# Kernel tuning notes

Measured on AMD Instinct MI355X. Metric: run time of the kernel, lower is better.

## Reference

```python
import jax, jax.numpy as jnp
import numpy as np

N = 50000          # num nodes
E = 800000         # num edges (before self loops)
F = 128            # input feature dim
UNITS = 128        # output units
ATT_UNITS = 128    # attention units (Q/K dim)
HEADS = 8


def setup_inputs() -> dict:
    key = jax.random.key(0)
    ks = jax.random.split(key, 6)
    s = 1.0 / np.sqrt(F).astype(np.float32)  # ~glorot scale
    return {
        "x": jax.random.normal(ks[0], (N, F), dtype=jnp.float32),
        "edge_index": jax.random.randint(ks[1], (2, E), 0, N, dtype=jnp.int32),
        "query_kernel": jax.random.normal(ks[2], (F, ATT_UNITS), dtype=jnp.float32) * s,
        "query_bias": jnp.zeros((ATT_UNITS,), jnp.float32),
        "key_kernel": jax.random.normal(ks[3], (F, ATT_UNITS), dtype=jnp.float32) * s,
        "key_bias": jnp.zeros((ATT_UNITS,), jnp.float32),
        "kernel": jax.random.normal(ks[4], (F, UNITS), dtype=jnp.float32) * s,
        "bias": jnp.zeros((UNITS,), jnp.float32),
    }


def segment_softmax(scores, seg, num_segments):
    # scores: [E', H], seg: [E'] -> softmax over edges sharing the same target node, per head
    smax = jax.ops.segment_max(scores, seg, num_segments=num_segments)
    sexp = jnp.exp(scores - smax[seg])
    ssum = jax.ops.segment_sum(sexp, seg, num_segments=num_segments)
    return sexp / ssum[seg]


def reference(x, edge_index, query_kernel, query_bias, key_kernel, key_bias, kernel, bias):
    num_nodes = x.shape[0]
    # add self-loop edges (as in tf_geometric add_self_loop_edge)
    loop = jnp.arange(num_nodes, dtype=edge_index.dtype)
    row = jnp.concatenate([edge_index[0], loop])  # target nodes, [E']
    col = jnp.concatenate([edge_index[1], loop])  # source nodes, [E']

    Q = jax.nn.relu(x @ query_kernel + query_bias)[row]  # [E', A]
    K = jax.nn.relu(x @ key_kernel + key_bias)[col]      # [E', A]
    V = (x @ kernel)[col]                                 # [E', U]

    # split into attention heads: tf.split(..., num_heads, axis=-1)
    Qh = Q.reshape(-1, HEADS, ATT_UNITS // HEADS)
    Kh = K.reshape(-1, HEADS, ATT_UNITS // HEADS)
    att = jnp.sum(Qh * Kh, axis=-1)                       # [E', H]
    alpha = segment_softmax(att, row, num_nodes)          # [E', H]

    # split_value_heads=True: split V into head slices, weight, scatter-add, concat
    Vh = V.reshape(-1, HEADS, UNITS // HEADS)             # [E', H, U/H]
    msg = Vh * alpha[:, :, None]
    out = jax.ops.segment_sum(msg, row, num_segments=num_nodes)  # [N, H, U/H]
    out = out.reshape(num_nodes, UNITS)
    out = out + bias  # use_bias=True, activation=None
    return out
```

## Files before the change

kernel.cpp:

```cpp
#include <hip/hip_runtime.h>
#include <hip/hip_fp16.h>
#include <cstdint>

#define FDIM 128
#define XSTR 136
#define NROWTILE 128
#define WCHUNKS ((FDIM * XSTR * 2) / 1024)
#define XCHUNKS ((NROWTILE * XSTR * 2) / 1024)
#define CSRS 128

typedef __attribute__((ext_vector_type(8))) _Float16 half8;
typedef __attribute__((ext_vector_type(2))) _Float16 h2;
typedef __attribute__((ext_vector_type(16))) float float16;

#if defined(__has_builtin)
#if __has_builtin(__builtin_amdgcn_fdot2)
#define HAVE_FDOT2 1
#endif
#endif

__device__ __forceinline__ void gload_lds16(const void* g, void* s) {
    __builtin_amdgcn_global_load_lds(
        (const __attribute__((address_space(1))) void*)g,
        (__attribute__((address_space(3))) void*)s, 16, 0, 0);
}

__device__ __forceinline__ h2 as_h2(unsigned u) {
    union { unsigned u; h2 h; } c; c.u = u; return c.h;
}
__device__ __forceinline__ float2 h2_to_f2(unsigned u) {
    __half2 h = *(__half2*)&u;
    return __half22float2(h);
}

__global__ __launch_bounds__(256) void edges_k(
    const float* __restrict__ x, __half* __restrict__ XH,
    const int* __restrict__ ei, int E,
    const float* __restrict__ Wq, const float* __restrict__ Wk,
    const float* __restrict__ Wv, __half* __restrict__ WTH,
    int* __restrict__ deg, int* __restrict__ csr, int N, int Npad)
{
    int idx = blockIdx.x * 256 + threadIdx.x;

    if (idx < Npad * 32) {
        int row = idx >> 5;
        int c = (idx & 31) << 2;
        float4 v = make_float4(0.f, 0.f, 0.f, 0.f);
        if (row < N) v = *(const float4*)(x + (size_t)row * FDIM + c);
        __half h[4] = {__float2half_rn(v.x), __float2half_rn(v.y),
                       __float2half_rn(v.z), __float2half_rn(v.w)};
        *(ushort4*)(XH + (size_t)row * XSTR + c) = *(ushort4*)h;
    }

    if (idx < 3 * FDIM * FDIM) {
        int mat = idx >> 14;
        int m = idx & 16383;
        int k = m >> 7;
        int nn = m & 127;
        const float* __restrict__ W = (mat == 0) ? Wq : (mat == 1) ? Wk : Wv;
        WTH[(size_t)mat * FDIM * XSTR + nn * XSTR + k] =
            __float2half_rn(W[k * FDIM + nn]);
    }

    if (idx < E) {
        int row = ei[idx];
        int col = ei[E + idx];
        int slot = atomicAdd(&deg[row], 1);
        if (slot < CSRS) csr[(row << 7) + slot] = col;
    }
}

__global__ __launch_bounds__(256) void gemm_mfma_k(
    const __half* __restrict__ XH, const __half* __restrict__ WTH,
    const float* __restrict__ bq, const float* __restrict__ bk,
    const float* __restrict__ bias,
    __half* __restrict__ Qb, uint2* __restrict__ KV, int N)
{
    __shared__ __half xs[NROWTILE * XSTR];
    __shared__ __half ws[FDIM * XSTR];

    const int tid  = threadIdx.x;
    const int wave = tid >> 6;
    const int lane = tid & 63;
    const int r0   = blockIdx.x * NROWTILE;
    const int mat  = blockIdx.y;

    const char* wbase = (const char*)(WTH + (size_t)mat * FDIM * XSTR);
    for (int c = wave; c < XCHUNKS; c += 4) {
        gload_lds16((const char*)(XH + (size_t)r0 * XSTR) + c * 1024 + lane * 16,
                    (char*)xs + c * 1024);
        gload_lds16(wbase + c * 1024 + lane * 16, (char*)ws + c * 1024);
    }
    __syncthreads();

    const int mrow = lane & 31;
    const int half = lane >> 5;
    const int arow = wave * 32 + mrow;

    float16 acc[4];
    #pragma unroll
    for (int nt = 0; nt < 4; ++nt)
        #pragma unroll
        for (int r = 0; r < 16; ++r) acc[nt][r] = 0.f;

    #pragma unroll
    for (int ks = 0; ks < 8; ++ks) {
        const int ko = ks * 16 + half * 8;
        half8 ah = *(const half8*)(xs + arow * XSTR + ko);
        #pragma unroll
        for (int nt = 0; nt < 4; ++nt) {
            half8 bh = *(const half8*)(ws + (nt * 32 + mrow) * XSTR + ko);
            acc[nt] = __builtin_amdgcn_mfma_f32_32x32x16_f16(ah, bh, acc[nt], 0, 0, 0);
        }
    }

    __syncthreads();

    const float* bvec = (mat == 0) ? bq : (mat == 1) ? bk : bias;
    #pragma unroll
    for (int nt = 0; nt < 4; ++nt) {
        const int col = nt * 32 + mrow;
        const float bb = bvec[col];
        #pragma unroll
        for (int reg = 0; reg < 16; ++reg) {
            int rl = wave * 32 + (reg & 3) + 8 * (reg >> 2) + 4 * half;
            float v = acc[nt][reg] + bb;
            if (mat < 2) v = fmaxf(v, 0.f);
            ws[rl * XSTR + col] = __float2half_rn(v);
        }
    }
    __syncthreads();

    if (mat == 0) {
        #pragma unroll
        for (int it = 0; it < 8; ++it) {
            int idx = it * 256 + tid;
            int row = idx >> 4;
            int c = (idx & 15) * 8;
            uint4 v = *(const uint4*)(ws + row * XSTR + c);
            if (r0 + row < N)
                *(uint4*)(Qb + (size_t)(r0 + row) * FDIM + c) = v;
        }
    } else {
        __half* kvh = (__half*)KV;
        const int sub = (mat == 2) ? 2 : 0;
        #pragma unroll
        for (int it = 0; it < 32; ++it) {
            int idx = it * 256 + tid;
            int row = idx >> 6;
            int p = idx & 63;
            unsigned v = *(const unsigned*)(ws + row * XSTR + 2 * p);
            if (r0 + row < N)
                *(unsigned*)(kvh + (size_t)(r0 + row) * 256 + p * 4 + sub) = v;
        }
    }
}

__global__ __launch_bounds__(256) void aggregate_k(
    const __half* __restrict__ Qb, const uint2* __restrict__ KV,
    const int* __restrict__ deg, const int* __restrict__ csr,
    float* __restrict__ out, int N)
{
    const int lane = threadIdx.x & 63;
    int n = blockIdx.x * 4 + (threadIdx.x >> 6);
    if (n >= N) return;
    n = __builtin_amdgcn_readfirstlane(n);

    int d = __builtin_amdgcn_readfirstlane(deg[n]);
    if (d > CSRS) d = CSRS;
    const int off   = n << 7;
    const int total = d + 1;

    const unsigned qu = *(const unsigned*)(Qb + (size_t)n * FDIM + 2 * lane);
    const h2 q2 = as_h2(qu);
#ifndef HAVE_FDOT2
    const float2 qf = h2_to_f2(qu);
#endif

    float acc0 = 0.f, acc1 = 0.f, lsum = 0.f;

    int idxbuf[8];
    #pragma unroll
    for (int u = 0; u < 8; ++u)
        idxbuf[u] = (u == 0) ? n : ((u < total) ? csr[off + u - 1] : 0);

    for (int t = 0; t < total; t += 8) {
        uint2 kv[8];
        #pragma unroll
        for (int u = 0; u < 8; ++u)
            kv[u] = KV[(((unsigned)idxbuf[u]) << 6) + lane];
        #pragma unroll
        for (int u = 0; u < 8; ++u) {
            int nx = t + 8 + u;
            idxbuf[u] = (nx < total) ? csr[off + nx - 1] : 0;
        }
        #pragma unroll
        for (int u = 0; u < 8; ++u) {
#ifdef HAVE_FDOT2
            float p = __builtin_amdgcn_fdot2(as_h2(kv[u].x), q2, 0.0f, false);
#else
            float2 kf = h2_to_f2(kv[u].x);
            float p = qf.x * kf.x + qf.y * kf.y;
#endif
            p += __shfl_xor(p, 1);
            p += __shfl_xor(p, 2);
            p += __shfl_xor(p, 4);
            float s = (t + u < total) ? __expf(p) : 0.f;
            float2 vf = h2_to_f2(kv[u].y);
            lsum += s;
            acc0 += s * vf.x;
            acc1 += s * vf.y;
        }
    }

    const float inv = 1.0f / lsum;
    float2 o;
    o.x = acc0 * inv;
    o.y = acc1 * inv;
    *(float2*)(out + (size_t)n * FDIM + 2 * lane) = o;
}

extern "C" void kernel_launch(void* const* d_in, const int* in_sizes, int n_in,
                              void* d_out, int out_size, void* d_ws, size_t ws_size,
                              hipStream_t stream)
{
    const float* x    = (const float*)d_in[0];
    const int*   ei   = (const int*)d_in[1];
    const float* Wq   = (const float*)d_in[2];
    const float* bq   = (const float*)d_in[3];
    const float* Wk   = (const float*)d_in[4];
    const float* bk   = (const float*)d_in[5];
    const float* Wv   = (const float*)d_in[6];
    const float* bias = (const float*)d_in[7];
    float* out = (float*)d_out;

    const int N = in_sizes[0] / FDIM;
    const int E = in_sizes[1] / 2;
    const int nblk = (N + NROWTILE - 1) / NROWTILE;
    const int Npad = nblk * NROWTILE;

    __half* WTH = (__half*)d_ws;
    __half* XH  = WTH + (size_t)3 * FDIM * XSTR;
    __half* Qb  = XH + (size_t)Npad * XSTR;
    uint2*  KV  = (uint2*)(Qb + (size_t)N * FDIM);
    int* deg    = (int*)(KV + (size_t)N * 64);
    int* csr    = deg + N;

    (void)hipMemsetAsync(deg, 0, (size_t)N * sizeof(int), stream);

    edges_k<<<(Npad * 32 + 255) / 256, 256, 0, stream>>>(
        x, XH, ei, E, Wq, Wk, Wv, WTH, deg, csr, N, Npad);

    gemm_mfma_k<<<dim3(nblk, 3), 256, 0, stream>>>(
        XH, WTH, bq, bk, bias, Qb, KV, N);

    aggregate_k<<<(N + 3) / 4, 256, 0, stream>>>(Qb, KV, deg, csr, out, N);
}
```

Before: 212.2 us.

## Fuse fp16 conversion of x into GEMM and loop over three weight matrices per block

Removes the separate XH half-precision staging buffer: each GEMM block now loads its fp32 x tile, converts it to fp16 in LDS, and computes Q, K and V in sequence, reloading each weight matrix into shared memory between passes. This reads x once instead of once per projection and drops the global write and readback of XH. In exchange the grid shrinks to a third as many blocks with serialized weight reloads and extra barriers, so there is less parallelism and weight-load latency is not overlapped with compute.

New measurement: 218.5 us. 3.0% more time.

```diff
diff --git a/kernel.cpp b/kernel.cpp
--- a/kernel.cpp
+++ b/kernel.cpp
@@ -6,7 +6,6 @@
 #define XSTR 136
 #define NROWTILE 128
 #define WCHUNKS ((FDIM * XSTR * 2) / 1024)
-#define XCHUNKS ((NROWTILE * XSTR * 2) / 1024)
 #define CSRS 128
 
 typedef __attribute__((ext_vector_type(8))) _Float16 half8;
@@ -34,23 +33,12 @@
 }
 
 __global__ __launch_bounds__(256) void edges_k(
-    const float* __restrict__ x, __half* __restrict__ XH,
     const int* __restrict__ ei, int E,
     const float* __restrict__ Wq, const float* __restrict__ Wk,
     const float* __restrict__ Wv, __half* __restrict__ WTH,
-    int* __restrict__ deg, int* __restrict__ csr, int N, int Npad)
+    int* __restrict__ deg, int* __restrict__ csr, int N)
 {
     int idx = blockIdx.x * 256 + threadIdx.x;
-
-    if (idx < Npad * 32) {
-        int row = idx >> 5;
-        int c = (idx & 31) << 2;
-        float4 v = make_float4(0.f, 0.f, 0.f, 0.f);
-        if (row < N) v = *(const float4*)(x + (size_t)row * FDIM + c);
-        __half h[4] = {__float2half_rn(v.x), __float2half_rn(v.y),
-                       __float2half_rn(v.z), __float2half_rn(v.w)};
-        *(ushort4*)(XH + (size_t)row * XSTR + c) = *(ushort4*)h;
-    }
 
     if (idx < 3 * FDIM * FDIM) {
         int mat = idx >> 14;
@@ -71,7 +59,7 @@
 }
 
 __global__ __launch_bounds__(256) void gemm_mfma_k(
-    const __half* __restrict__ XH, const __half* __restrict__ WTH,
+    const float* __restrict__ x, const __half* __restrict__ WTH,
     const float* __restrict__ bq, const float* __restrict__ bk,
     const float* __restrict__ bias,
     __half* __restrict__ Qb, uint2* __restrict__ KV, int N)
@@ -83,75 +71,92 @@
     const int wave = tid >> 6;
     const int lane = tid & 63;
     const int r0   = blockIdx.x * NROWTILE;
-    const int mat  = blockIdx.y;
-
-    const char* wbase = (const char*)(WTH + (size_t)mat * FDIM * XSTR);
-    for (int c = wave; c < XCHUNKS; c += 4) {
-        gload_lds16((const char*)(XH + (size_t)r0 * XSTR) + c * 1024 + lane * 16,
-                    (char*)xs + c * 1024);
-        gload_lds16(wbase + c * 1024 + lane * 16, (char*)ws + c * 1024);
-    }
-    __syncthreads();
+
+    for (int c = wave; c < WCHUNKS; c += 4)
+        gload_lds16((const char*)WTH + c * 1024 + lane * 16, (char*)ws + c * 1024);
+
+    #pragma unroll
+    for (int it = 0; it < 16; ++it) {
+        int idx = it * 256 + tid;
+        int row = idx >> 5;
+        int c = (idx & 31) << 2;
+        float4 v = make_float4(0.f, 0.f, 0.f, 0.f);
+        if (r0 + row < N) v = *(const float4*)(x + (size_t)(r0 + row) * FDIM + c);
+        __half h[4] = {__float2half_rn(v.x), __float2half_rn(v.y),
+                       __float2half_rn(v.z), __float2half_rn(v.w)};
+        *(ushort4*)(xs + row * XSTR + c) = *(ushort4*)h;
+    }
 
     const int mrow = lane & 31;
     const int half = lane >> 5;
     const int arow = wave * 32 + mrow;
 
-    float16 acc[4];
-    #pragma unroll
-    for (int nt = 0; nt < 4; ++nt)
-        #pragma unroll
-        for (int r = 0; r < 16; ++r) acc[nt][r] = 0.f;
-
-    #pragma unroll
-    for (int ks = 0; ks < 8; ++ks) {
-        const int ko = ks * 16 + half * 8;
-        half8 ah = *(const half8*)(xs + arow * XSTR + ko);
+    for (int mat = 0; mat < 3; ++mat) {
+        __syncthreads();
+
+        float16 acc[4];
+        #pragma unroll
+        for (int nt = 0; nt < 4; ++nt)
+            #pragma unroll
+            for (int r = 0; r < 16; ++r) acc[nt][r] = 0.f;
+
+        #pragma unroll
+        for (int ks = 0; ks < 8; ++ks) {
+            const int ko = ks * 16 + half * 8;
+            half8 ah = *(const half8*)(xs + arow * XSTR + ko);
+            #pragma unroll
+            for (int nt = 0; nt < 4; ++nt) {
+                half8 bh = *(const half8*)(ws + (nt * 32 + mrow) * XSTR + ko);
+                acc[nt] = __builtin_amdgcn_mfma_f32_32x32x16_f16(ah, bh, acc[nt], 0, 0, 0);
+            }
+        }
+
+        __syncthreads();
+
+        const float* bvec = (mat == 0) ? bq : (mat == 1) ? bk : bias;
         #pragma unroll
         for (int nt = 0; nt < 4; ++nt) {
-            half8 bh = *(const half8*)(ws + (nt * 32 + mrow) * XSTR + ko);
-            acc[nt] = __builtin_amdgcn_mfma_f32_32x32x16_f16(ah, bh, acc[nt], 0, 0, 0);
-        }
-    }
-
-    __syncthreads();
-
-    const float* bvec = (mat == 0) ? bq : (mat == 1) ? bk : bias;
-    #pragma unroll
-    for (int nt = 0; nt < 4; ++nt) {
-        const int col = nt * 32 + mrow;
-        const float bb = bvec[col];
-        #pragma unroll
-        for (int reg = 0; reg < 16; ++reg) {
-            int rl = wave * 32 + (reg & 3) + 8 * (reg >> 2) + 4 * half;
-            float v = acc[nt][reg] + bb;
-            if (mat < 2) v = fmaxf(v, 0.f);
-            ws[rl * XSTR + col] = __float2half_rn(v);
-        }
-    }
-    __syncthreads();
-
-    if (mat == 0) {
-        #pragma unroll
-        for (int it = 0; it < 8; ++it) {
-            int idx = it * 256 + tid;
-            int row = idx >> 4;
-            int c = (idx & 15) * 8;
-            uint4 v = *(const uint4*)(ws + row * XSTR + c);
-            if (r0 + row < N)
-                *(uint4*)(Qb + (size_t)(r0 + row) * FDIM + c) = v;
-        }
-    } else {
-        __half* kvh = (__half*)KV;
-        const int sub = (mat == 2) ? 2 : 0;
-        #pragma unroll
-        for (int it = 0; it < 32; ++it) {
-            int idx = it * 256 + tid;
-            int row = idx >> 6;
-            int p = idx & 63;
-            unsigned v = *(const unsigned*)(ws + row * XSTR + 2 * p);
-            if (r0 + row < N)
-                *(unsigned*)(kvh + (size_t)(r0 + row) * 256 + p * 4 + sub) = v;
+            const int col = nt * 32 + mrow;
+            const float bb = bvec[col];
+            #pragma unroll
+            for (int reg = 0; reg < 16; ++reg) {
+                int rl = wave * 32 + (reg & 3) + 8 * (reg >> 2) + 4 * half;
+                float v = acc[nt][reg] + bb;
+                if (mat < 2) v = fmaxf(v, 0.f);
+                ws[rl * XSTR + col] = __float2half_rn(v);
+            }
+        }
+        __syncthreads();
+
+        if (mat == 0) {
+            #pragma unroll
+            for (int it = 0; it < 8; ++it) {
+                int idx = it * 256 + tid;
+                int row = idx >> 4;
+                int c = (idx & 15) * 8;
+                uint4 v = *(const uint4*)(ws + row * XSTR + c);
+                if (r0 + row < N)
+                    *(uint4*)(Qb + (size_t)(r0 + row) * FDIM + c) = v;
+            }
+        } else {
+            __half* kvh = (__half*)KV;
+            const int sub = (mat == 2) ? 2 : 0;
+            #pragma unroll
+            for (int it = 0; it < 32; ++it) {
+                int idx = it * 256 + tid;
+                int row = idx >> 6;
+                int p = idx & 63;
+                unsigned v = *(const unsigned*)(ws + row * XSTR + 2 * p);
+                if (r0 + row < N)
+                    *(unsigned*)(kvh + (size_t)(r0 + row) * 256 + p * 4 + sub) = v;
+            }
+        }
+        __syncthreads();
+
+        if (mat < 2) {
+            const char* wbase = (const char*)(WTH + (size_t)(mat + 1) * FDIM * XSTR);
+            for (int c = wave; c < WCHUNKS; c += 4)
+                gload_lds16(wbase + c * 1024 + lane * 16, (char*)ws + c * 1024);
         }
     }
 }
@@ -237,22 +242,20 @@
     const int N = in_sizes[0] / FDIM;
     const int E = in_sizes[1] / 2;
     const int nblk = (N + NROWTILE - 1) / NROWTILE;
-    const int Npad = nblk * NROWTILE;
 
     __half* WTH = (__half*)d_ws;
-    __half* XH  = WTH + (size_t)3 * FDIM * XSTR;
-    __half* Qb  = XH + (size_t)Npad * XSTR;
+    __half* Qb  = WTH + (size_t)3 * FDIM * XSTR;
     uint2*  KV  = (uint2*)(Qb + (size_t)N * FDIM);
     int* deg    = (int*)(KV + (size_t)N * 64);
     int* csr    = deg + N;
 
     (void)hipMemsetAsync(deg, 0, (size_t)N * sizeof(int), stream);
 
-    edges_k<<<(Npad * 32 + 255) / 256, 256, 0, stream>>>(
-        x, XH, ei, E, Wq, Wk, Wv, WTH, deg, csr, N, Npad);
-
-    gemm_mfma_k<<<dim3(nblk, 3), 256, 0, stream>>>(
-        XH, WTH, bq, bk, bias, Qb, KV, N);
+    edges_k<<<(E + 255) / 256, 256, 0, stream>>>(
+        ei, E, Wq, Wk, Wv, WTH, deg, csr, N);
+
+    gemm_mfma_k<<<nblk, 256, 0, stream>>>(
+        x, WTH, bq, bk, bias, Qb, KV, N);
 
     aggregate_k<<<(N + 3) / 4, 256, 0, stream>>>(Qb, KV, deg, csr, out, N);
 }
```
